# Optimization experiments

Measured on AMD Instinct MI355X. Metric: run time of the kernel, lower is better.

## Reference

```python
import jax, jax.numpy as jnp
import numpy as np

N_EMBD = 384
NUM_HEADS = 6
HEAD_SIZE = 64


def setup_inputs() -> dict:
    key = jax.random.key(0)
    k1, k2, k3, k4 = jax.random.split(key, 4)
    B, T = 32, 1024
    x = jax.random.normal(k1, (B, T, N_EMBD), dtype=jnp.float32)
    # torch Linear(n_embd, 3*n_embd, bias=False): store as [in, out]
    s_attn = 1.0 / np.sqrt(N_EMBD)
    W_attn = jax.random.uniform(k2, (N_EMBD, 3 * N_EMBD), dtype=jnp.float32, minval=-s_attn, maxval=s_attn)
    W_proj = jax.random.uniform(k3, (N_EMBD, N_EMBD), dtype=jnp.float32, minval=-s_attn, maxval=s_attn)
    b_proj = jax.random.uniform(k4, (N_EMBD,), dtype=jnp.float32, minval=-s_attn, maxval=s_attn)
    return {"x": x, "W_attn": W_attn, "W_proj": W_proj, "b_proj": b_proj}


def reference(x, W_attn, W_proj, b_proj):
    B, T, C = x.shape
    H, D = NUM_HEADS, HEAD_SIZE
    qkv = x @ W_attn                      # [B, T, 3C]
    q, k, v = jnp.split(qkv, 3, axis=2)   # each [B, T, C]
    # [B, H, T, D]
    q = q.reshape(B, T, H, D).transpose(0, 2, 1, 3)
    k = k.reshape(B, T, H, D).transpose(0, 2, 1, 3)
    v = v.reshape(B, T, H, D).transpose(0, 2, 1, 3)
    scale = 1.0 / jnp.sqrt(jnp.asarray(D, dtype=x.dtype))
    scores = jnp.einsum("bhqd,bhkd->bhqk", q, k) * scale  # [B, H, T, T]
    causal = jnp.tril(jnp.ones((T, T), dtype=bool))
    scores = jnp.where(causal, scores, jnp.asarray(-jnp.inf, dtype=scores.dtype))
    attn = jax.nn.softmax(scores, axis=-1)
    y = jnp.einsum("bhqk,bhkd->bhqd", attn, v)             # [B, H, T, D]
    y = y.transpose(0, 2, 1, 3).reshape(B, T, C)
    # dropout is inactive in eval mode
    return y @ W_proj + b_proj
```

## Files before the change

### kernel.cpp

```cpp
#include <hip/hip_runtime.h>
#include <hip/hip_bf16.h>

#define DEV __device__ __forceinline__

typedef __attribute__((ext_vector_type(4))) float f32x4;
typedef __bf16 bf16x8 __attribute__((ext_vector_type(8)));

static DEV unsigned short f2bf(float f) {
    union { float f; unsigned u; } x; x.f = f;
    unsigned r = x.u + 0x7fffu + ((x.u >> 16) & 1u);
    return (unsigned short)(r >> 16);
}

static DEV f32x4 zero4() { f32x4 v; v[0] = 0.f; v[1] = 0.f; v[2] = 0.f; v[3] = 0.f; return v; }

#define GL1(p) ((const __attribute__((address_space(1))) void*)(p))
#define LDS3(p) ((__attribute__((address_space(3))) void*)(p))


__global__ __launch_bounds__(256) void k_prep(
    const float* __restrict__ x, unsigned short* __restrict__ xb,
    const float* __restrict__ Wa, unsigned short* __restrict__ WaT,
    const float* __restrict__ Wp, unsigned short* __restrict__ WpT)
{
    int i = blockIdx.x * 256 + threadIdx.x;
    if (i < 3145728) {
        float4 v = reinterpret_cast<const float4*>(x)[i];
        ushort4 o;
        o.x = f2bf(v.x); o.y = f2bf(v.y); o.z = f2bf(v.z); o.w = f2bf(v.w);
        reinterpret_cast<ushort4*>(xb)[i] = o;
    } else if (i < 3145728 + 442368) {
        int j = i - 3145728;
        int n = j / 384, k = j - n * 384;
        WaT[j] = f2bf(Wa[(size_t)k * 1152 + n]);
    } else if (i < 3145728 + 442368 + 147456) {
        int j = i - (3145728 + 442368);
        int n = j / 384, k = j - n * 384;
        WpT[j] = f2bf(Wp[(size_t)k * 384 + n]);
    }
}


template <int SWAP>
static DEV void gemm_mainloop(
    const unsigned short* __restrict__ A,
    const unsigned short* __restrict__ B,
    int m0, int n0, int tid,
    f32x4 (&acc)[4][4],
    unsigned short (&lA)[128][64], unsigned short (&lB)[128][64])
{
    const int K = 384;
    const int w = tid >> 6, lane = tid & 63;
    const int wm = (w >> 1) * 64, wn = (w & 1) * 64;
    const int lr = lane & 15, lg = lane >> 4;
    const int lrow = lane >> 3;
    const int lcol = ((lane & 7) ^ lrow) * 8;

    for (int kb = 0; kb < K; kb += 64) {
        __syncthreads();
#pragma unroll
        for (int c = 0; c < 4; ++c) {
            int rb = (w * 4 + c) * 8;
            __builtin_amdgcn_global_load_lds(GL1(&A[(size_t)(m0 + rb + lrow) * K + kb + lcol]),
                                             LDS3(&lA[rb][0]), 16, 0, 0);
            __builtin_amdgcn_global_load_lds(GL1(&B[(size_t)(n0 + rb + lrow) * K + kb + lcol]),
                                             LDS3(&lB[rb][0]), 16, 0, 0);
        }
        __syncthreads();

        bf16x8 af[4][2], bfr[4][2];
#pragma unroll
        for (int kc = 0; kc < 2; ++kc) {
#pragma unroll
            for (int t = 0; t < 4; ++t) {
                int ga = ((kc * 4 + lg) ^ (lr & 7)) * 8;
                af[t][kc]  = *(const bf16x8*)&lA[wm + t * 16 + lr][ga];
                bfr[t][kc] = *(const bf16x8*)&lB[wn + t * 16 + lr][ga];
            }
        }
#pragma unroll
        for (int kc = 0; kc < 2; ++kc)
#pragma unroll
            for (int mt = 0; mt < 4; ++mt)
#pragma unroll
                for (int nt = 0; nt < 4; ++nt)
                    acc[mt][nt] = SWAP
                        ? __builtin_amdgcn_mfma_f32_16x16x32_bf16(bfr[nt][kc], af[mt][kc], acc[mt][nt], 0, 0, 0)
                        : __builtin_amdgcn_mfma_f32_16x16x32_bf16(af[mt][kc], bfr[nt][kc], acc[mt][nt], 0, 0, 0);
    }
}


__global__ __launch_bounds__(256) void k_gemm_qkv(
    const unsigned short* __restrict__ A,
    const unsigned short* __restrict__ B,
    unsigned short* __restrict__ Qb, unsigned short* __restrict__ Kb,
    unsigned short* __restrict__ Vb)
{
    __shared__ unsigned short lA[128][64];
    __shared__ unsigned short lB[128][64];

    const int tid = threadIdx.x;
    const int m0 = blockIdx.x * 128, n0 = blockIdx.y * 128;
    const int w = tid >> 6, lane = tid & 63;
    const int wm = (w >> 1) * 64, wn = (w & 1) * 64;
    const int lr = lane & 15, lg = lane >> 4;

    f32x4 acc[4][4];
#pragma unroll
    for (int i = 0; i < 4; i++)
#pragma unroll
        for (int j = 0; j < 4; j++) acc[i][j] = zero4();

    if (blockIdx.y < 6) {
        gemm_mainloop<1>(A, B, m0, n0, tid, acc, lA, lB);
        const int which = blockIdx.y / 3;
#pragma unroll
        for (int mt = 0; mt < 4; ++mt) {
            int row = m0 + wm + mt * 16 + lr;
            int bb = row >> 10, tloc = row & 1023;
#pragma unroll
            for (int nt = 0; nt < 4; ++nt) {
                int col = n0 + wn + nt * 16 + lg * 4;
                int c = col - which * 384;
                int hh = c >> 6, d0 = c & 63;
                size_t bh = (size_t)bb * 6 + hh;
                int kc = (d0 >> 5) & 1;
                int ln = (tloc & 15) + 16 * ((d0 >> 3) & 3);
                int e0 = d0 & 7;
                union { __bf16 h4[4]; uint2 u; } pk;
                if (which == 0) {
#pragma unroll
                    for (int r = 0; r < 4; ++r)
                        pk.h4[r] = (__bf16)(acc[mt][nt][r] * 0.18033688f);
                    int qt = tloc >> 5, fmt = (tloc >> 4) & 1;
                    *(uint2*)&Qb[((((bh * 32 + qt) * 2 + fmt) * 2 + kc) * 64 + ln) * 8 + e0] = pk.u;
                } else {
#pragma unroll
                    for (int r = 0; r < 4; ++r)
                        pk.h4[r] = (__bf16)acc[mt][nt][r];
                    int ktt = tloc >> 6, fnt = (tloc >> 4) & 3;
                    *(uint2*)&Kb[((((bh * 16 + ktt) * 4 + fnt) * 2 + kc) * 64 + ln) * 8 + e0] = pk.u;
                }
            }
        }
    } else {
        gemm_mainloop<0>(A, B, m0, n0, tid, acc, lA, lB);
#pragma unroll
        for (int nt = 0; nt < 4; ++nt) {
            int col = n0 + wn + nt * 16 + lr;
            int c = col - 768;
            int hh = c >> 6, d = c & 63;
            int fnt = d >> 4;
#pragma unroll
            for (int mt = 0; mt < 4; ++mt) {
                int row0 = m0 + wm + mt * 16 + lg * 4;
                int bb = row0 >> 10, t0 = row0 & 1023;
                size_t bh = (size_t)bb * 6 + hh;
                int ktt = t0 >> 6, kc = (t0 >> 5) & 1, e0 = t0 & 7;
                int ln = (d & 15) + 16 * ((t0 >> 3) & 3);
                union { __bf16 h4[4]; uint2 u; } pk;
#pragma unroll
                for (int r = 0; r < 4; ++r)
                    pk.h4[r] = (__bf16)acc[mt][nt][r];
                *(uint2*)&Vb[((((bh * 16 + ktt) * 4 + fnt) * 2 + kc) * 64 + ln) * 8 + e0] = pk.u;
            }
        }
    }
}


__global__ __launch_bounds__(256) void k_gemm_proj(
    const unsigned short* __restrict__ A,
    const unsigned short* __restrict__ B,
    const float* __restrict__ bias, float* __restrict__ Out)
{
    __shared__ unsigned short lA[128][64];
    __shared__ unsigned short lB[128][64];

    const int tid = threadIdx.x;
    const int m0 = blockIdx.x * 128, n0 = blockIdx.y * 128;
    const int w = tid >> 6, lane = tid & 63;
    const int wm = (w >> 1) * 64, wn = (w & 1) * 64;
    const int lr = lane & 15, lg = lane >> 4;

    f32x4 acc[4][4];
#pragma unroll
    for (int i = 0; i < 4; i++)
#pragma unroll
        for (int j = 0; j < 4; j++) acc[i][j] = zero4();

    gemm_mainloop<1>(A, B, m0, n0, tid, acc, lA, lB);

#pragma unroll
    for (int mt = 0; mt < 4; ++mt) {
        int row = m0 + wm + mt * 16 + lr;
#pragma unroll
        for (int nt = 0; nt < 4; ++nt) {
            int col = n0 + wn + nt * 16 + lg * 4;
            f32x4 bv = *(const f32x4*)&bias[col];
            f32x4 ov;
#pragma unroll
            for (int r = 0; r < 4; ++r) ov[r] = acc[mt][nt][r] + bv[r];
            *(f32x4*)&Out[(size_t)row * 384 + col] = ov;
        }
    }
}


template <int NTM, bool MASK>
static DEV void attn_tile(
    const unsigned short* lKt, const unsigned short* lVt, unsigned short* lPw,
    const bf16x8 (&qf)[2][2], f32x4 (&o)[2][4], float (&ls)[2],
    int kt, int qw, int lane)
{
    constexpr int KCM = NTM / 2;
    const int lr = lane & 15, lg = lane >> 4;

    bf16x8 kf[NTM][2];
#pragma unroll
    for (int nt = 0; nt < NTM; ++nt)
#pragma unroll
        for (int kc = 0; kc < 2; ++kc)
            kf[nt][kc] = *(const bf16x8*)&lKt[(nt * 2 + kc) * 512 + lane * 8];

    bf16x8 vf[4][KCM];
#pragma unroll
    for (int nt = 0; nt < 4; ++nt)
#pragma unroll
        for (int kc = 0; kc < KCM; ++kc)
            vf[nt][kc] = *(const bf16x8*)&lVt[(nt * 2 + kc) * 512 + lane * 8];

    f32x4 st[2][NTM];
#pragma unroll
    for (int mt = 0; mt < 2; ++mt)
#pragma unroll
        for (int nt = 0; nt < NTM; ++nt) st[mt][nt] = zero4();

    __builtin_amdgcn_s_setprio(1);
#pragma unroll
    for (int kc = 0; kc < 2; ++kc)
#pragma unroll
        for (int mt = 0; mt < 2; ++mt)
#pragma unroll
            for (int nt = 0; nt < NTM; ++nt)
                st[mt][nt] = __builtin_amdgcn_mfma_f32_16x16x32_bf16(kf[nt][kc], qf[mt][kc], st[mt][nt], 0, 0, 0);
    __builtin_amdgcn_s_setprio(0);

#pragma unroll
    for (int mt = 0; mt < 2; ++mt) {
#pragma unroll
        for (int nt = 0; nt < NTM; ++nt) {
            union { __bf16 hh[4]; uint2 u; } pk;
            float e[4];
#pragma unroll
            for (int r = 0; r < 4; ++r) {
                float ev = __builtin_amdgcn_exp2f(st[mt][nt][r]);
                if (MASK) {
                    int kg = kt * 64 + nt * 16 + lg * 4 + r;
                    int qg = qw + mt * 16 + lr;
                    if (kg > qg) ev = 0.f;
                }
                e[r] = ev;
                pk.hh[r] = (__bf16)ev;
            }
            ls[mt] += (e[0] + e[1]) + (e[2] + e[3]);
            int ln2 = lr + 16 * ((nt & 1) * 2 + (lg >> 1));
            *(uint2*)&lPw[(mt * 2 + (nt >> 1)) * 512 + ln2 * 8 + (lg & 1) * 4] = pk.u;
        }
    }

    bf16x8 pf[2][KCM];
#pragma unroll
    for (int mt = 0; mt < 2; ++mt)
#pragma unroll
        for (int kc = 0; kc < KCM; ++kc)
            pf[mt][kc] = *(const bf16x8*)&lPw[(mt * 2 + kc) * 512 + lane * 8];

    __builtin_amdgcn_s_setprio(1);
#pragma unroll
    for (int mt = 0; mt < 2; ++mt)
#pragma unroll
        for (int nt = 0; nt < 4; ++nt)
#pragma unroll
            for (int kc = 0; kc < KCM; ++kc)
                o[mt][nt] = __builtin_amdgcn_mfma_f32_16x16x32_bf16(vf[nt][kc], pf[mt][kc], o[mt][nt], 0, 0, 0);
    __builtin_amdgcn_s_setprio(0);
}

static DEV void attn_pass(
    int gg, int w, int lane, int b, int h, int bh,
    const unsigned short* __restrict__ Qf,
    const unsigned short* __restrict__ Kbh,
    const unsigned short* __restrict__ Vbh,
    unsigned short* __restrict__ Y,
    unsigned short (&lK)[2][4096], unsigned short (&lV)[2][4096],
    unsigned short* lPw)
{
    const int lr = lane & 15, lg = lane >> 4;
    const int qt = 4 * gg + w;
    const int qw = qt * 32;
    const int nkt = qt / 2 + 1;
    const int nsteps = 2 * gg + 2;

    bf16x8 qf[2][2];
#pragma unroll
    for (int mt = 0; mt < 2; ++mt)
#pragma unroll
        for (int kc = 0; kc < 2; ++kc)
            qf[mt][kc] = *(const bf16x8*)&Qf[((((size_t)bh * 32 + qt) * 2 + mt) * 2 + kc) * 512 + lane * 8];

    f32x4 o[2][4];
    float ls[2] = {0.f, 0.f};
#pragma unroll
    for (int mt = 0; mt < 2; ++mt)
#pragma unroll
        for (int nt = 0; nt < 4; ++nt) o[mt][nt] = zero4();

    __syncthreads();

#pragma unroll
    for (int i = 0; i < 2; ++i) {
        __builtin_amdgcn_global_load_lds(GL1(Kbh + (size_t)w * 1024 + i * 512 + lane * 8),
                                         LDS3(&lK[0][w * 1024 + i * 512]), 16, 0, 0);
        __builtin_amdgcn_global_load_lds(GL1(Vbh + (size_t)w * 1024 + i * 512 + lane * 8),
                                         LDS3(&lV[0][w * 1024 + i * 512]), 16, 0, 0);
    }

    for (int kt = 0; kt < nsteps; ++kt) {
        __syncthreads();
        if (kt + 1 < nsteps) {
            int nb = (kt + 1) & 1;
#pragma unroll
            for (int i = 0; i < 2; ++i) {
                __builtin_amdgcn_global_load_lds(GL1(Kbh + (size_t)(kt + 1) * 4096 + w * 1024 + i * 512 + lane * 8),
                                                 LDS3(&lK[nb][w * 1024 + i * 512]), 16, 0, 0);
                __builtin_amdgcn_global_load_lds(GL1(Vbh + (size_t)(kt + 1) * 4096 + w * 1024 + i * 512 + lane * 8),
                                                 LDS3(&lV[nb][w * 1024 + i * 512]), 16, 0, 0);
            }
        }
        if (kt < nkt) {
            const unsigned short* lKt = lK[kt & 1];
            const unsigned short* lVt = lV[kt & 1];
            if (kt == nkt - 1) {
                if (qt & 1) attn_tile<4, true>(lKt, lVt, lPw, qf, o, ls, kt, qw, lane);
                else        attn_tile<2, true>(lKt, lVt, lPw, qf, o, ls, kt, qw, lane);
            } else {
                attn_tile<4, false>(lKt, lVt, lPw, qf, o, ls, kt, qw, lane);
            }
        }
    }

    float inv[2];
#pragma unroll
    for (int mt = 0; mt < 2; ++mt) {
        float s = ls[mt];
        s += __shfl_xor(s, 16);
        s += __shfl_xor(s, 32);
        inv[mt] = 1.0f / s;
    }
#pragma unroll
    for (int mt = 0; mt < 2; ++mt) {
#pragma unroll
        for (int nt = 0; nt < 4; ++nt) {
            union { __bf16 h4[4]; uint2 u; } pk;
#pragma unroll
            for (int r = 0; r < 4; ++r) pk.h4[r] = (__bf16)(o[mt][nt][r] * inv[mt]);
            *(uint2*)&Y[((size_t)b * 1024 + qw + mt * 16 + lr) * 384 + h * 64 + nt * 16 + lg * 4] = pk.u;
        }
    }
}

__global__ __launch_bounds__(256, 3) void k_attn(
    const unsigned short* __restrict__ Qf,
    const unsigned short* __restrict__ Kf,
    const unsigned short* __restrict__ Vf,
    unsigned short* __restrict__ Y)
{
    __shared__ unsigned short lK[2][4096];
    __shared__ unsigned short lV[2][4096];
    __shared__ unsigned short lPf[4][2048];

    const int tid = threadIdx.x;
    const int w = tid >> 6, lane = tid & 63;
    const int bh = blockIdx.x;
    const int g = blockIdx.y;
    const int b = bh / 6, h = bh - b * 6;

    const unsigned short* Kbh = Kf + (size_t)bh * 65536;
    const unsigned short* Vbh = Vf + (size_t)bh * 65536;

    attn_pass(g,     w, lane, b, h, bh, Qf, Kbh, Vbh, Y, lK, lV, lPf[w]);
    attn_pass(7 - g, w, lane, b, h, bh, Qf, Kbh, Vbh, Y, lK, lV, lPf[w]);
}


extern "C" void kernel_launch(void* const* d_in, const int* in_sizes, int n_in,
                              void* d_out, int out_size, void* d_ws, size_t ws_size,
                              hipStream_t stream)
{
    const float* x  = (const float*)d_in[0];
    const float* Wa = (const float*)d_in[1];
    const float* Wp = (const float*)d_in[2];
    const float* bp = (const float*)d_in[3];
    float* out = (float*)d_out;

    char* ws = (char*)d_ws;
    unsigned short* xb  = (unsigned short*)(ws);
    unsigned short* WaT = (unsigned short*)(ws + 25165824);
    unsigned short* WpT = (unsigned short*)(ws + 26050560);
    unsigned short* Qb  = (unsigned short*)(ws + 26345472);
    unsigned short* Kb  = (unsigned short*)(ws + 51511296);
    unsigned short* Vtb = (unsigned short*)(ws + 76677120);

    k_prep<<<14592, 256, 0, stream>>>(x, xb, Wa, WaT, Wp, WpT);
    k_gemm_qkv<<<dim3(256, 9), 256, 0, stream>>>(xb, WaT, Qb, Kb, Vtb);
    k_attn<<<dim3(192, 4), 256, 0, stream>>>(Qb, Kb, Vtb, xb);
    k_gemm_proj<<<dim3(256, 3), 256, 0, stream>>>(xb, WpT, bp, out);
}
```

Baseline: 124.8 us.

## Use 256-row QKV GEMM tiles with 512 threads and N-fastest block order

The QKV projection GEMM now uses 512-thread blocks covering 256 rows by 128 columns. Eight waves share one B tile, which halves B reloads per output, and the grid is reordered so the N tiles vary fastest. This lets consecutive blocks reuse the same A rows through L2. The projection GEMM grid is swapped in the same way for A-row locality. The larger LDS footprint and thread count may reduce occupancy per CU.

```diff
diff --git a/kernel.cpp b/kernel.cpp
--- a/kernel.cpp
+++ b/kernel.cpp
@@ -42,6 +42,59 @@
 
 
 template <int SWAP>
+static DEV void gemm_mainloop512(
+    const unsigned short* __restrict__ A,
+    const unsigned short* __restrict__ B,
+    int m0, int n0, int tid,
+    f32x4 (&acc)[4][4],
+    unsigned short (&lA)[256][64], unsigned short (&lB)[128][64])
+{
+    const int K = 384;
+    const int w = tid >> 6, lane = tid & 63;
+    const int wm = (w >> 1) * 64, wn = (w & 1) * 64;
+    const int lr = lane & 15, lg = lane >> 4;
+    const int lrow = lane >> 3;
+    const int lcol = ((lane & 7) ^ lrow) * 8;
+
+    for (int kb = 0; kb < K; kb += 64) {
+        __syncthreads();
+#pragma unroll
+        for (int c = 0; c < 4; ++c) {
+            int rb = w * 32 + c * 8;
+            __builtin_amdgcn_global_load_lds(GL1(&A[(size_t)(m0 + rb + lrow) * K + kb + lcol]),
+                                             LDS3(&lA[rb][0]), 16, 0, 0);
+        }
+#pragma unroll
+        for (int c = 0; c < 2; ++c) {
+            int rb = w * 16 + c * 8;
+            __builtin_amdgcn_global_load_lds(GL1(&B[(size_t)(n0 + rb + lrow) * K + kb + lcol]),
+                                             LDS3(&lB[rb][0]), 16, 0, 0);
+        }
+        __syncthreads();
+
+        bf16x8 af[4][2], bfr[4][2];
+#pragma unroll
+        for (int kc = 0; kc < 2; ++kc) {
+#pragma unroll
+            for (int t = 0; t < 4; ++t) {
+                int ga = ((kc * 4 + lg) ^ (lr & 7)) * 8;
+                af[t][kc]  = *(const bf16x8*)&lA[wm + t * 16 + lr][ga];
+                bfr[t][kc] = *(const bf16x8*)&lB[wn + t * 16 + lr][ga];
+            }
+        }
+#pragma unroll
+        for (int kc = 0; kc < 2; ++kc)
+#pragma unroll
+            for (int mt = 0; mt < 4; ++mt)
+#pragma unroll
+                for (int nt = 0; nt < 4; ++nt)
+                    acc[mt][nt] = SWAP
+                        ? __builtin_amdgcn_mfma_f32_16x16x32_bf16(bfr[nt][kc], af[mt][kc], acc[mt][nt], 0, 0, 0)
+                        : __builtin_amdgcn_mfma_f32_16x16x32_bf16(af[mt][kc], bfr[nt][kc], acc[mt][nt], 0, 0, 0);
+    }
+}
+
+template <int SWAP>
 static DEV void gemm_mainloop(
     const unsigned short* __restrict__ A,
     const unsigned short* __restrict__ B,
@@ -91,17 +144,18 @@
 }
 
 
-__global__ __launch_bounds__(256) void k_gemm_qkv(
+__global__ __launch_bounds__(512) void k_gemm_qkv(
     const unsigned short* __restrict__ A,
     const unsigned short* __restrict__ B,
     unsigned short* __restrict__ Qb, unsigned short* __restrict__ Kb,
     unsigned short* __restrict__ Vb)
 {
-    __shared__ unsigned short lA[128][64];
+    __shared__ unsigned short lA[256][64];
     __shared__ unsigned short lB[128][64];
 
     const int tid = threadIdx.x;
-    const int m0 = blockIdx.x * 128, n0 = blockIdx.y * 128;
+    const int bx = blockIdx.x;
+    const int m0 = blockIdx.y * 256, n0 = bx * 128;
     const int w = tid >> 6, lane = tid & 63;
     const int wm = (w >> 1) * 64, wn = (w & 1) * 64;
     const int lr = lane & 15, lg = lane >> 4;
@@ -112,9 +166,9 @@
 #pragma unroll
         for (int j = 0; j < 4; j++) acc[i][j] = zero4();
 
-    if (blockIdx.y < 6) {
-        gemm_mainloop<1>(A, B, m0, n0, tid, acc, lA, lB);
-        const int which = blockIdx.y / 3;
+    if (bx < 6) {
+        gemm_mainloop512<1>(A, B, m0, n0, tid, acc, lA, lB);
+        const int which = bx / 3;
 #pragma unroll
         for (int mt = 0; mt < 4; ++mt) {
             int row = m0 + wm + mt * 16 + lr;
@@ -145,7 +199,7 @@
             }
         }
     } else {
-        gemm_mainloop<0>(A, B, m0, n0, tid, acc, lA, lB);
+        gemm_mainloop512<0>(A, B, m0, n0, tid, acc, lA, lB);
 #pragma unroll
         for (int nt = 0; nt < 4; ++nt) {
             int col = n0 + wn + nt * 16 + lr;
@@ -179,7 +233,7 @@
     __shared__ unsigned short lB[128][64];
 
     const int tid = threadIdx.x;
-    const int m0 = blockIdx.x * 128, n0 = blockIdx.y * 128;
+    const int m0 = blockIdx.y * 128, n0 = blockIdx.x * 128;
     const int w = tid >> 6, lane = tid & 63;
     const int wm = (w >> 1) * 64, wn = (w & 1) * 64;
     const int lr = lane & 15, lg = lane >> 4;
@@ -414,7 +468,7 @@
     unsigned short* Vtb = (unsigned short*)(ws + 76677120);
 
     k_prep<<<14592, 256, 0, stream>>>(x, xb, Wa, WaT, Wp, WpT);
-    k_gemm_qkv<<<dim3(256, 9), 256, 0, stream>>>(xb, WaT, Qb, Kb, Vtb);
+    k_gemm_qkv<<<dim3(9, 128), 512, 0, stream>>>(xb, WaT, Qb, Kb, Vtb);
     k_attn<<<dim3(192, 4), 256, 0, stream>>>(Qb, Kb, Vtb, xb);
-    k_gemm_proj<<<dim3(256, 3), 256, 0, stream>>>(xb, WpT, bp, out);
-}
+    k_gemm_proj<<<dim3(3, 256), 256, 0, stream>>>(xb, WpT, bp, out);
+}
```

Result: slower. 140.3 us (+12.4%).
